# Performance work log

Hardware: AMD Instinct MI355X
Metric: run time of the kernel (lower is better)

Reference implementation:

```python
import jax, jax.numpy as jnp
import numpy as np

B, N, C, H = 4, 1024, 1024, 16
D = C // H  # head_dim = 64


def setup_inputs() -> dict:
    key = jax.random.key(0)
    k1, k2, k3 = jax.random.split(key, 3)
    x = jax.random.normal(k1, (B, N, C), dtype=jnp.float32)
    Wqkv = jax.random.normal(k2, (3 * C, C), dtype=jnp.float32) * (C ** -0.5)
    Wproj = jax.random.normal(k3, (C, C), dtype=jnp.float32) * (C ** -0.5)
    bproj = jnp.zeros((C,), dtype=jnp.float32)
    epoch = 25  # selects mask_2 (window w=8) per the original branching
    return {"x": x, "Wqkv": Wqkv, "Wproj": Wproj, "bproj": bproj, "epoch": epoch}


def _band_mask(n, w):
    # get_attn_mask(N, w) == (|i - j| <= w) for every row (boundary cases included)
    idx = jnp.arange(n)
    return jnp.abs(idx[:, None] - idx[None, :]) <= w


def reference(x, Wqkv, Wproj, bproj, epoch):
    b, n, c = x.shape
    d = c // H
    # qkv linear (no bias), then the module's per-head interleaved split:
    # view(B,N,H,3d) -> permute(B,H,N,3d) -> tensor_split into q,k,v
    qkv = jnp.einsum('bnc,oc->bno', x, Wqkv)            # [B,N,3C]
    qkv = qkv.reshape(b, n, H, 3 * d).transpose(0, 2, 1, 3)  # [B,H,N,3d]
    q, k, v = jnp.split(qkv, 3, axis=-1)                # each [B,H,N,d]
    scale = d ** -0.5
    score = jnp.einsum('bhid,bhjd->bhij', q, k) * scale  # [B,H,N,N]
    if epoch is not None and epoch < 50:
        if epoch < 20:
            w = 6
        elif epoch < 30:
            w = 8
        elif epoch < 40:
            w = 10
        else:
            w = 12
        mask = _band_mask(n, w)  # [N,N] bool
        score = jnp.where(mask[None, None], score, jnp.float32(-1e9))
    attn = jax.nn.softmax(score, axis=-1)
    ctx = jnp.einsum('bhij,bhjd->bhid', attn, v)         # [B,H,N,d]
    ctx = ctx.transpose(0, 2, 1, 3).reshape(b, n, c)     # [B,N,C]
    out = jnp.einsum('bnc,oc->bno', ctx, Wproj) + bproj
    return out
```

## Files before the change

### kernel.cpp

```cpp
#include <hip/hip_runtime.h>
#include <hip/hip_bf16.h>


typedef __bf16 bf16x8_t __attribute__((ext_vector_type(8)));
typedef unsigned short u16x8_t __attribute__((ext_vector_type(8)));
typedef float f32x4_t __attribute__((ext_vector_type(4)));

__device__ __forceinline__ void load_lds16(const void* g, void* l) {
    __builtin_amdgcn_global_load_lds(
        (__attribute__((address_space(1))) void*)(g),
        (__attribute__((address_space(3))) void*)(l),
        16, 0, 0);
}

__device__ __forceinline__ u16x8_t cvt8(float4 u, float4 v) {
    union { u16x8_t p; __hip_bfloat16 h[8]; } w;
    w.h[0] = __float2bfloat16(u.x); w.h[1] = __float2bfloat16(u.y);
    w.h[2] = __float2bfloat16(u.z); w.h[3] = __float2bfloat16(u.w);
    w.h[4] = __float2bfloat16(v.x); w.h[5] = __float2bfloat16(v.y);
    w.h[6] = __float2bfloat16(v.z); w.h[7] = __float2bfloat16(v.w);
    return w.p;
}

__global__ __launch_bounds__(512, 2) void gemm1_qkv(
    const float* __restrict__ A,
    const float* __restrict__ B,
    __hip_bfloat16* __restrict__ C)
{
    __shared__ __align__(16) char smem[114688];
    const int tid = threadIdx.x;

    const int orig = blockIdx.y * 16 + blockIdx.x;
    const int xcd = orig & 7, slot = orig >> 3;
    const int hi = slot >> 4;
    const int s  = xcd * 2 + hi;
    const int w  = slot & 15;
    const int m0 = ((s & 3) * 4 + (w & 3)) * 256;
    const int n0 = ((s >> 2) * 4 + (w >> 2)) * 192;

    const int wave = tid >> 6, lane = tid & 63;
    const int wr = wave >> 2, wc = wave & 3;
    const int lr = lane & 15, kg = lane >> 4;
    const int K = 1024, Nn = 3072;

    const int qa0 = tid, qa1 = tid + 512;
    const int qb0 = tid, qb1 = tid + 256;
    const int ra0 = qa0 >> 2, ca0 = ((qa0 & 3) ^ ((ra0 >> 1) & 3)) * 8;
    const int ra1 = qa1 >> 2, ca1 = ((qa1 & 3) ^ ((ra1 >> 1) & 3)) * 8;
    const int rb0 = qb0 >> 2, cb0 = ((qb0 & 3) ^ ((rb0 >> 1) & 3)) * 8;
    const int rb1 = qb1 >> 2, cb1 = ((qb1 & 3) ^ ((rb1 >> 1) & 3)) * 8;
    const float* Ap0 = A + (size_t)(m0 + ra0) * K + ca0;
    const float* Ap1 = A + (size_t)(m0 + ra1) * K + ca1;
    const float* Bp0 = B + (size_t)(n0 + rb0) * K + cb0;
    const float* Bp1 = B + (size_t)(n0 + rb1) * K + cb1;
    const bool bextra = (tid >= 256);

    float4 a00 = {}, a01 = {}, a10 = {}, a11 = {};
    float4 b00 = {}, b01 = {}, b10 = {}, b11 = {};

#define LOADR(t) { const int ko_ = (t) * 32;                                   \
    a00 = *(const float4*)(Ap0 + ko_); a01 = *(const float4*)(Ap0 + ko_ + 4);  \
    a10 = *(const float4*)(Ap1 + ko_); a11 = *(const float4*)(Ap1 + ko_ + 4);  \
    b00 = *(const float4*)(Bp0 + ko_); b01 = *(const float4*)(Bp0 + ko_ + 4);  \
    if (bextra) { b10 = *(const float4*)(Bp1 + ko_);                           \
                  b11 = *(const float4*)(Bp1 + ko_ + 4); } }
#define WRITE(t) { char* d_ = smem + ((t) & 3) * 28672;                        \
    *(u16x8_t*)(d_ + qa0 * 16) = cvt8(a00, a01);                               \
    *(u16x8_t*)(d_ + qa1 * 16) = cvt8(a10, a11);                               \
    *(u16x8_t*)(d_ + 16384 + qb0 * 16) = cvt8(b00, b01);                       \
    if (bextra) *(u16x8_t*)(d_ + 16384 + qb1 * 16) = cvt8(b10, b11); }

    f32x4_t acc[8][3] = {};
    const int rsw = ((kg ^ ((lr >> 1) & 3)) * 16);
    const int arow = wr * 128 + lr;
    const int brow = wc * 48 + lr;

    LOADR(0); WRITE(0);
    LOADR(1); WRITE(1);
    LOADR(2);
    __syncthreads();

    for (int t = 0; t < 32; ++t) {
        const int sb_ = (t & 3) * 28672;
        bf16x8_t a_[8], b_[3];
#pragma unroll
        for (int mi = 0; mi < 8; ++mi)
            a_[mi] = *(const bf16x8_t*)(smem + sb_ + (arow + mi * 16) * 64 + rsw);
#pragma unroll
        for (int ni = 0; ni < 3; ++ni)
            b_[ni] = *(const bf16x8_t*)(smem + sb_ + 16384 + (brow + ni * 16) * 64 + rsw);
        if (t < 30) WRITE(t + 2);
        if (t < 29) LOADR(t + 3);
        __builtin_amdgcn_s_setprio(1);
#pragma unroll
        for (int mi = 0; mi < 8; ++mi)
#pragma unroll
            for (int ni = 0; ni < 3; ++ni)
                acc[mi][ni] = __builtin_amdgcn_mfma_f32_16x16x32_bf16(
                    a_[mi], b_[ni], acc[mi][ni], 0, 0, 0);
        __builtin_amdgcn_s_setprio(0);
        __syncthreads();
    }
#undef LOADR
#undef WRITE

    __hip_bfloat16* cl = (__hip_bfloat16*)smem;
#pragma unroll
    for (int mi = 0; mi < 8; ++mi)
#pragma unroll
        for (int ni = 0; ni < 3; ++ni)
#pragma unroll
            for (int r = 0; r < 4; ++r)
                cl[(wr * 128 + mi * 16 + kg * 4 + r) * 200 + wc * 48 + ni * 16 + lr] =
                    __float2bfloat16(acc[mi][ni][r]);
    __syncthreads();
#pragma unroll
    for (int c = 0; c < 12; ++c) {
        const int id = tid + c * 512;
        const int row = id / 24, cc = id - row * 24;
        f32x4_t v = *(const f32x4_t*)(smem + row * 400 + cc * 16);
        *(f32x4_t*)((char*)C + ((size_t)(m0 + row) * Nn + n0) * 2 + cc * 16) = v;
    }
}

__global__ __launch_bounds__(512, 2) void gemm2_proj(
    const __hip_bfloat16* __restrict__ A,
    const float* __restrict__ B,
    float* __restrict__ C,
    const float* __restrict__ bias)
{
    __shared__ __align__(16) char smem[65536];
    const int tid = threadIdx.x;
    const int orig = blockIdx.y * 8 + blockIdx.x;
    const int wgid = (orig & 7) * 32 + (orig >> 3);
    const int m0 = (wgid >> 3) * 128, n0 = (wgid & 7) * 128;

    const int wave = tid >> 6, lane = tid & 63;
    const int wr = wave >> 2, wc = wave & 3;
    const int lr = lane & 15, kg = lane >> 4;
    const int K = 1024, Nn = 1024;

    const int q = tid;
    const int row = q >> 2, cw = ((q & 3) ^ ((row >> 1) & 3)) * 8;
    const __hip_bfloat16* Ap = A + (size_t)(m0 + row) * K + cw;
    const float*          Bp = B + (size_t)(n0 + row) * K + cw;

    float4 av = {}, bv0 = {}, bv1 = {};

#define LOADR2(t) { const int ko_ = (t) * 32;                                  \
    av  = *(const float4*)(Ap + ko_);                        \
    bv0 = *(const float4*)(Bp + ko_); bv1 = *(const float4*)(Bp + ko_ + 4); }
#define WRITE2(t) { char* d_ = smem + ((t) & 3) * 16384;                       \
    *(float4*)(d_ + q * 16) = av;                                              \
    *(u16x8_t*)(d_ + 8192 + q * 16) = cvt8(bv0, bv1); }

    f32x4_t acc[4][2] = {};
    const int rsw = ((kg ^ ((lr >> 1) & 3)) * 16);
    const int arow = wr * 64 + lr;
    const int brow = wc * 32 + lr;

    LOADR2(0); WRITE2(0);
    LOADR2(1); WRITE2(1);
    LOADR2(2);
    __syncthreads();

    for (int t = 0; t < 32; ++t) {
        const int sb_ = (t & 3) * 16384;
        bf16x8_t a_[4], b_[2];
#pragma unroll
        for (int mi = 0; mi < 4; ++mi)
            a_[mi] = *(const bf16x8_t*)(smem + sb_ + (arow + mi * 16) * 64 + rsw);
#pragma unroll
        for (int ni = 0; ni < 2; ++ni)
            b_[ni] = *(const bf16x8_t*)(smem + sb_ + 8192 + (brow + ni * 16) * 64 + rsw);
        if (t < 30) WRITE2(t + 2);
        if (t < 29) LOADR2(t + 3);
        __builtin_amdgcn_s_setprio(1);
#pragma unroll
        for (int mi = 0; mi < 4; ++mi)
#pragma unroll
            for (int ni = 0; ni < 2; ++ni)
                acc[mi][ni] = __builtin_amdgcn_mfma_f32_16x16x32_bf16(
                    a_[mi], b_[ni], acc[mi][ni], 0, 0, 0);
        __builtin_amdgcn_s_setprio(0);
        __syncthreads();
    }
#undef LOADR2
#undef WRITE2

    float* cf = (float*)smem;
#pragma unroll
    for (int p = 0; p < 2; ++p) {
        if (p) __syncthreads();
        if (wr == p) {
#pragma unroll
            for (int mi = 0; mi < 4; ++mi)
#pragma unroll
                for (int ni = 0; ni < 2; ++ni) {
                    const int scol = wc * 32 + ni * 16 + lr;
#pragma unroll
                    for (int r = 0; r < 4; ++r)
                        cf[(mi * 16 + kg * 4 + r) * 132 + scol] = acc[mi][ni][r];
                }
        }
        __syncthreads();
#pragma unroll
        for (int cc = 0; cc < 4; ++cc) {
            const int chunk = tid + cc * 512;
            const int srow = chunk >> 5;
            const int sc = (chunk & 31) * 4;
            f32x4_t v = *(const f32x4_t*)(smem + srow * 528 + sc * 4);
            const f32x4_t bv = *(const f32x4_t*)(bias + n0 + sc);
            v += bv;
            *(f32x4_t*)(C + (size_t)(m0 + p * 64 + srow) * Nn + n0 + sc) = v;
        }
    }
}

__global__ __launch_bounds__(256) void attn_band_mfma(
    const __hip_bfloat16* __restrict__ qkv,
    __hip_bfloat16* __restrict__ ctx,
    const int* __restrict__ epoch_ptr)
{
    __shared__ __align__(16) __hip_bfloat16 K_lds[128 * 64];
    __shared__ __align__(16) __hip_bfloat16 V_lds[64 * 136];
    __shared__ __hip_bfloat16 P_lds[4][16 * 40];

    const int tid = threadIdx.x;
    const int wave = tid >> 6, lane = tid & 63;
    const int lr = lane & 15, kg = lane >> 4;

    const int bid = blockIdx.x;
    const int tg = bid & 15;
    const int bh = bid >> 4;
    const int h = bh & 15, b = bh >> 4;
    const int base = tg * 64;
    const int i0 = base + wave * 16;

    const int e = *epoch_ptr;
    int w;
    if      (e < 20) w = 6;
    else if (e < 30) w = 8;
    else if (e < 40) w = 10;
    else if (e < 50) w = 12;
    else             w = 1023;

    const size_t rowb = (size_t)b * 1024;
    const int hq = h * 192;

#pragma unroll
    for (int it = 0; it < 4; ++it) {
        const int q = tid + it * 256;
        const int row = q >> 3, s = q & 7;
        const int c = s ^ (row & 7);
        int gk = base - 32 + row;
        gk = gk < 0 ? 0 : (gk > 1023 ? 1023 : gk);
        load_lds16(qkv + (rowb + gk) * 3072 + hq + 64 + c * 8,
                   (char*)K_lds + q * 16);
    }
    {
        const int pr = tid & 63, dg = tid >> 6;
        int gk0 = base - 32 + 2 * pr, gk1 = gk0 + 1;
        gk0 = gk0 < 0 ? 0 : (gk0 > 1023 ? 1023 : gk0);
        gk1 = gk1 < 0 ? 0 : (gk1 > 1023 ? 1023 : gk1);
        const __hip_bfloat16* v0 = qkv + (rowb + gk0) * 3072 + hq + 128 + dg * 16;
        const __hip_bfloat16* v1 = qkv + (rowb + gk1) * 3072 + hq + 128 + dg * 16;
        u16x8_t a0 = *(const u16x8_t*)v0, b0 = *(const u16x8_t*)(v0 + 8);
        u16x8_t a1 = *(const u16x8_t*)v1, b1 = *(const u16x8_t*)(v1 + 8);
#pragma unroll
        for (int c2 = 0; c2 < 8; ++c2) {
            *(unsigned int*)&V_lds[(dg * 16 + c2) * 136 + 2 * pr] =
                (unsigned int)a0[c2] | ((unsigned int)a1[c2] << 16);
            *(unsigned int*)&V_lds[(dg * 16 + 8 + c2) * 136 + 2 * pr] =
                (unsigned int)b0[c2] | ((unsigned int)b1[c2] << 16);
        }
    }

    bf16x8_t aq[2];
#pragma unroll
    for (int ks = 0; ks < 2; ++ks)
        aq[ks] = *(const bf16x8_t*)(qkv + (rowb + i0 + lr) * 3072 + hq + ks * 32 + kg * 8);

    __syncthreads();

    float m[4] = {-1e30f, -1e30f, -1e30f, -1e30f};
    float l[4] = {0.f, 0.f, 0.f, 0.f};
    f32x4_t o[4] = {};

    int jlo = i0 - w;      if (jlo < 0) jlo = 0;
    int jhi = i0 + 15 + w; if (jhi > 1023) jhi = 1023;
    const int t0 = (base >> 5) - 1;

    for (int p = (jlo >> 5); p <= (jhi >> 5); ++p) {
        const int kb = p * 32;
        const int tl = p - t0;

        f32x4_t s2[2] = {};
#pragma unroll
        for (int t = 0; t < 2; ++t)
#pragma unroll
            for (int ks = 0; ks < 2; ++ks) {
                const int lkr = tl * 32 + t * 16 + lr;
                bf16x8_t bk = *(const bf16x8_t*)(
                    (char*)K_lds + lkr * 128 + (((ks * 4 + kg) ^ (lr & 7)) * 16));
                s2[t] = __builtin_amdgcn_mfma_f32_16x16x32_bf16(aq[ks], bk, s2[t], 0, 0, 0);
            }

        float sv[2][4];
#pragma unroll
        for (int t = 0; t < 2; ++t)
#pragma unroll
            for (int r = 0; r < 4; ++r) {
                const int qi = i0 + kg * 4 + r;
                const int j  = kb + t * 16 + lr;
                int d = qi - j; if (d < 0) d = -d;
                sv[t][r] = (d <= w) ? s2[t][r] * 0.125f : -1e30f;
            }

        float tm[4];
#pragma unroll
        for (int r = 0; r < 4; ++r) tm[r] = fmaxf(sv[0][r], sv[1][r]);
#pragma unroll
        for (int msk = 1; msk < 16; msk <<= 1)
#pragma unroll
            for (int r = 0; r < 4; ++r) tm[r] = fmaxf(tm[r], __shfl_xor(tm[r], msk));

        float sc[4], ps[4], pvv[2][4];
#pragma unroll
        for (int r = 0; r < 4; ++r) {
            const float mn = fmaxf(m[r], tm[r]);
            sc[r] = __expf(m[r] - mn);
            pvv[0][r] = __expf(sv[0][r] - mn);
            pvv[1][r] = __expf(sv[1][r] - mn);
            ps[r] = pvv[0][r] + pvv[1][r];
            m[r] = mn;
        }
#pragma unroll
        for (int msk = 1; msk < 16; msk <<= 1)
#pragma unroll
            for (int r = 0; r < 4; ++r) ps[r] += __shfl_xor(ps[r], msk);
#pragma unroll
        for (int r = 0; r < 4; ++r) l[r] = l[r] * sc[r] + ps[r];
#pragma unroll
        for (int ni = 0; ni < 4; ++ni)
#pragma unroll
            for (int r = 0; r < 4; ++r) o[ni][r] *= sc[r];

#pragma unroll
        for (int t = 0; t < 2; ++t)
#pragma unroll
            for (int r = 0; r < 4; ++r)
                P_lds[wave][(kg * 4 + r) * 40 + t * 16 + lr] =
                    __float2bfloat16(pvv[t][r]);

        bf16x8_t ap = *(const bf16x8_t*)&P_lds[wave][lr * 40 + kg * 8];
#pragma unroll
        for (int ni = 0; ni < 4; ++ni) {
            bf16x8_t bv = *(const bf16x8_t*)&V_lds[(ni * 16 + lr) * 136 + tl * 32 + kg * 8];
            o[ni] = __builtin_amdgcn_mfma_f32_16x16x32_bf16(ap, bv, o[ni], 0, 0, 0);
        }
    }

#pragma unroll
    for (int ni = 0; ni < 4; ++ni)
#pragma unroll
        for (int r = 0; r < 4; ++r)
            ctx[(rowb + i0 + kg * 4 + r) * 1024 + h * 64 + ni * 16 + lr] =
                __float2bfloat16(o[ni][r] / l[r]);
}

extern "C" void kernel_launch(void* const* d_in, const int* in_sizes, int n_in,
                              void* d_out, int out_size, void* d_ws, size_t ws_size,
                              hipStream_t stream)
{
    const float* x     = (const float*)d_in[0];
    const float* Wqkv  = (const float*)d_in[1];
    const float* Wproj = (const float*)d_in[2];
    const float* bproj = (const float*)d_in[3];
    const int*   epoch = (const int*)d_in[4];

    char* ws = (char*)d_ws;
    __hip_bfloat16* qkvb = (__hip_bfloat16*)(ws);
    __hip_bfloat16* ctxb = (__hip_bfloat16*)(ws + 25165824);

    gemm1_qkv<<<dim3(16, 16), 512, 0, stream>>>(x, Wqkv, qkvb);

    attn_band_mfma<<<1024, 256, 0, stream>>>(qkvb, ctxb, epoch);

    gemm2_proj<<<dim3(8, 32), 512, 0, stream>>>(
        ctxb, Wproj, (float*)d_out, bproj);
}
```

Before: 68.05 us.

## Double K-tile depth to 64 in both GEMMs with double-buffered LDS

Both GEMM kernels now stage K-tiles of 64 instead of 32. The LDS ring goes from four stages to two, with an 8-way XOR swizzle over 128-byte rows, and each tile is consumed in two 32-wide MFMA sub-steps. This halves the number of __syncthreads barriers and main-loop iterations and issues larger batches of global loads, at the cost of more registers held for prefetched data and a shallower prefetch pipeline. The projection output store also becomes nontemporal.

Result: slower. 83.91 us (+23.3%).

```diff
diff --git a/kernel.cpp b/kernel.cpp
--- a/kernel.cpp
+++ b/kernel.cpp
@@ -43,62 +43,68 @@
     const int lr = lane & 15, kg = lane >> 4;
     const int K = 1024, Nn = 3072;
 
-    const int qa0 = tid, qa1 = tid + 512;
-    const int qb0 = tid, qb1 = tid + 256;
-    const int ra0 = qa0 >> 2, ca0 = ((qa0 & 3) ^ ((ra0 >> 1) & 3)) * 8;
-    const int ra1 = qa1 >> 2, ca1 = ((qa1 & 3) ^ ((ra1 >> 1) & 3)) * 8;
-    const int rb0 = qb0 >> 2, cb0 = ((qb0 & 3) ^ ((rb0 >> 1) & 3)) * 8;
-    const int rb1 = qb1 >> 2, cb1 = ((qb1 & 3) ^ ((rb1 >> 1) & 3)) * 8;
-    const float* Ap0 = A + (size_t)(m0 + ra0) * K + ca0;
-    const float* Ap1 = A + (size_t)(m0 + ra1) * K + ca1;
-    const float* Bp0 = B + (size_t)(n0 + rb0) * K + cb0;
-    const float* Bp1 = B + (size_t)(n0 + rb1) * K + cb1;
-    const bool bextra = (tid >= 256);
-
-    float4 a00 = {}, a01 = {}, a10 = {}, a11 = {};
-    float4 b00 = {}, b01 = {}, b10 = {}, b11 = {};
-
-#define LOADR(t) { const int ko_ = (t) * 32;                                   \
-    a00 = *(const float4*)(Ap0 + ko_); a01 = *(const float4*)(Ap0 + ko_ + 4);  \
-    a10 = *(const float4*)(Ap1 + ko_); a11 = *(const float4*)(Ap1 + ko_ + 4);  \
-    b00 = *(const float4*)(Bp0 + ko_); b01 = *(const float4*)(Bp0 + ko_ + 4);  \
-    if (bextra) { b10 = *(const float4*)(Bp1 + ko_);                           \
-                  b11 = *(const float4*)(Bp1 + ko_ + 4); } }
-#define WRITE(t) { char* d_ = smem + ((t) & 3) * 28672;                        \
-    *(u16x8_t*)(d_ + qa0 * 16) = cvt8(a00, a01);                               \
-    *(u16x8_t*)(d_ + qa1 * 16) = cvt8(a10, a11);                               \
-    *(u16x8_t*)(d_ + 16384 + qb0 * 16) = cvt8(b00, b01);                       \
-    if (bextra) *(u16x8_t*)(d_ + 16384 + qb1 * 16) = cvt8(b10, b11); }
+    const float* ApP[4];
+    const float* BpP[3];
+#pragma unroll
+    for (int i = 0; i < 4; ++i) {
+        const int q = tid + i * 512, row = q >> 3, c = (q & 7) ^ (row & 7);
+        ApP[i] = A + (size_t)(m0 + row) * K + c * 8;
+    }
+#pragma unroll
+    for (int i = 0; i < 3; ++i) {
+        const int q = tid + i * 512, row = q >> 3, c = (q & 7) ^ (row & 7);
+        BpP[i] = B + (size_t)(n0 + row) * K + c * 8;
+    }
+
+    float4 sa[4][2], sb[3][2];
+
+#define LOADR(t) { const int ko_ = (t) * 64;                                    \
+    _Pragma("unroll") for (int i = 0; i < 4; ++i) {                             \
+        sa[i][0] = *(const float4*)(ApP[i] + ko_);                              \
+        sa[i][1] = *(const float4*)(ApP[i] + ko_ + 4); }                        \
+    _Pragma("unroll") for (int i = 0; i < 3; ++i) {                             \
+        sb[i][0] = *(const float4*)(BpP[i] + ko_);                              \
+        sb[i][1] = *(const float4*)(BpP[i] + ko_ + 4); } }
+#define WRITE(t) { char* d_ = smem + ((t) & 1) * 57344;                         \
+    _Pragma("unroll") for (int i = 0; i < 4; ++i)                               \
+        *(u16x8_t*)(d_ + (tid + i * 512) * 16) = cvt8(sa[i][0], sa[i][1]);      \
+    _Pragma("unroll") for (int i = 0; i < 3; ++i)                               \
+        *(u16x8_t*)(d_ + 32768 + (tid + i * 512) * 16) = cvt8(sb[i][0], sb[i][1]); }
 
     f32x4_t acc[8][3] = {};
-    const int rsw = ((kg ^ ((lr >> 1) & 3)) * 16);
     const int arow = wr * 128 + lr;
     const int brow = wc * 48 + lr;
 
     LOADR(0); WRITE(0);
-    LOADR(1); WRITE(1);
-    LOADR(2);
+    LOADR(1);
     __syncthreads();
 
-    for (int t = 0; t < 32; ++t) {
-        const int sb_ = (t & 3) * 28672;
-        bf16x8_t a_[8], b_[3];
-#pragma unroll
-        for (int mi = 0; mi < 8; ++mi)
-            a_[mi] = *(const bf16x8_t*)(smem + sb_ + (arow + mi * 16) * 64 + rsw);
-#pragma unroll
-        for (int ni = 0; ni < 3; ++ni)
-            b_[ni] = *(const bf16x8_t*)(smem + sb_ + 16384 + (brow + ni * 16) * 64 + rsw);
-        if (t < 30) WRITE(t + 2);
-        if (t < 29) LOADR(t + 3);
-        __builtin_amdgcn_s_setprio(1);
-#pragma unroll
-        for (int mi = 0; mi < 8; ++mi)
+    for (int t = 0; t < 16; ++t) {
+        const int sb_ = (t & 1) * 57344;
+#pragma unroll
+        for (int ks = 0; ks < 2; ++ks) {
+            const int ch = ((kg + ks * 4) ^ (lr & 7)) * 16;
+            bf16x8_t aF[8], bF[3];
+#pragma unroll
+            for (int mi = 0; mi < 8; ++mi)
+                aF[mi] = *(const bf16x8_t*)(smem + sb_ + (arow + mi * 16) * 128 + ch);
 #pragma unroll
             for (int ni = 0; ni < 3; ++ni)
-                acc[mi][ni] = __builtin_amdgcn_mfma_f32_16x16x32_bf16(
-                    a_[mi], b_[ni], acc[mi][ni], 0, 0, 0);
-        __builtin_amdgcn_s_setprio(0);
+                bF[ni] = *(const bf16x8_t*)(smem + sb_ + 32768 + (brow + ni * 16) * 128 + ch);
+            if (ks == 0) {
+                if (t < 15) WRITE(t + 1);
+            } else {
+                if (t < 14) LOADR(t + 2);
+            }
+            __builtin_amdgcn_s_setprio(1);
+#pragma unroll
+            for (int mi = 0; mi < 8; ++mi)
+#pragma unroll
+                for (int ni = 0; ni < 3; ++ni)
+                    acc[mi][ni] = __builtin_amdgcn_mfma_f32_16x16x32_bf16(
+                        aF[mi], bF[ni], acc[mi][ni], 0, 0, 0);
+            __builtin_amdgcn_s_setprio(0);
+        }
         __syncthreads();
     }
 #undef LOADR
@@ -140,49 +146,61 @@
     const int lr = lane & 15, kg = lane >> 4;
     const int K = 1024, Nn = 1024;
 
-    const int q = tid;
-    const int row = q >> 2, cw = ((q & 3) ^ ((row >> 1) & 3)) * 8;
-    const __hip_bfloat16* Ap = A + (size_t)(m0 + row) * K + cw;
-    const float*          Bp = B + (size_t)(n0 + row) * K + cw;
-
-    float4 av = {}, bv0 = {}, bv1 = {};
-
-#define LOADR2(t) { const int ko_ = (t) * 32;                                  \
-    av  = *(const float4*)(Ap + ko_);                        \
-    bv0 = *(const float4*)(Bp + ko_); bv1 = *(const float4*)(Bp + ko_ + 4); }
-#define WRITE2(t) { char* d_ = smem + ((t) & 3) * 16384;                       \
-    *(float4*)(d_ + q * 16) = av;                                              \
-    *(u16x8_t*)(d_ + 8192 + q * 16) = cvt8(bv0, bv1); }
+    const __hip_bfloat16* ApP[2];
+    const float* BpP[2];
+#pragma unroll
+    for (int i = 0; i < 2; ++i) {
+        const int q = tid + i * 512, row = q >> 3, c = (q & 7) ^ (row & 7);
+        ApP[i] = A + (size_t)(m0 + row) * K + c * 8;
+        BpP[i] = B + (size_t)(n0 + row) * K + c * 8;
+    }
+
+    float4 sa[2], sbl[2][2];
+
+#define LOADR2(t) { const int ko_ = (t) * 64;                                   \
+    _Pragma("unroll") for (int i = 0; i < 2; ++i) {                             \
+        sa[i] = *(const float4*)(ApP[i] + ko_);                                 \
+        sbl[i][0] = *(const float4*)(BpP[i] + ko_);                             \
+        sbl[i][1] = *(const float4*)(BpP[i] + ko_ + 4); } }
+#define WRITE2(t) { char* d_ = smem + ((t) & 1) * 32768;                        \
+    _Pragma("unroll") for (int i = 0; i < 2; ++i) {                             \
+        *(float4*)(d_ + (tid + i * 512) * 16) = sa[i];                          \
+        *(u16x8_t*)(d_ + 16384 + (tid + i * 512) * 16) = cvt8(sbl[i][0], sbl[i][1]); } }
 
     f32x4_t acc[4][2] = {};
-    const int rsw = ((kg ^ ((lr >> 1) & 3)) * 16);
     const int arow = wr * 64 + lr;
     const int brow = wc * 32 + lr;
 
     LOADR2(0); WRITE2(0);
-    LOADR2(1); WRITE2(1);
-    LOADR2(2);
+    LOADR2(1);
     __syncthreads();
 
-    for (int t = 0; t < 32; ++t) {
-        const int sb_ = (t & 3) * 16384;
-        bf16x8_t a_[4], b_[2];
-#pragma unroll
-        for (int mi = 0; mi < 4; ++mi)
-            a_[mi] = *(const bf16x8_t*)(smem + sb_ + (arow + mi * 16) * 64 + rsw);
-#pragma unroll
-        for (int ni = 0; ni < 2; ++ni)
-            b_[ni] = *(const bf16x8_t*)(smem + sb_ + 8192 + (brow + ni * 16) * 64 + rsw);
-        if (t < 30) WRITE2(t + 2);
-        if (t < 29) LOADR2(t + 3);
-        __builtin_amdgcn_s_setprio(1);
-#pragma unroll
-        for (int mi = 0; mi < 4; ++mi)
+    for (int t = 0; t < 16; ++t) {
+        const int sb_ = (t & 1) * 32768;
+#pragma unroll
+        for (int ks = 0; ks < 2; ++ks) {
+            const int ch = ((kg + ks * 4) ^ (lr & 7)) * 16;
+            bf16x8_t aF[4], bF[2];
+#pragma unroll
+            for (int mi = 0; mi < 4; ++mi)
+                aF[mi] = *(const bf16x8_t*)(smem + sb_ + (arow + mi * 16) * 128 + ch);
 #pragma unroll
             for (int ni = 0; ni < 2; ++ni)
-                acc[mi][ni] = __builtin_amdgcn_mfma_f32_16x16x32_bf16(
-                    a_[mi], b_[ni], acc[mi][ni], 0, 0, 0);
-        __builtin_amdgcn_s_setprio(0);
+                bF[ni] = *(const bf16x8_t*)(smem + sb_ + 16384 + (brow + ni * 16) * 128 + ch);
+            if (ks == 0) {
+                if (t < 15) WRITE2(t + 1);
+            } else {
+                if (t < 14) LOADR2(t + 2);
+            }
+            __builtin_amdgcn_s_setprio(1);
+#pragma unroll
+            for (int mi = 0; mi < 4; ++mi)
+#pragma unroll
+                for (int ni = 0; ni < 2; ++ni)
+                    acc[mi][ni] = __builtin_amdgcn_mfma_f32_16x16x32_bf16(
+                        aF[mi], bF[ni], acc[mi][ni], 0, 0, 0);
+            __builtin_amdgcn_s_setprio(0);
+        }
         __syncthreads();
     }
 #undef LOADR2
@@ -212,7 +230,8 @@
             f32x4_t v = *(const f32x4_t*)(smem + srow * 528 + sc * 4);
             const f32x4_t bv = *(const f32x4_t*)(bias + n0 + sc);
             v += bv;
-            *(f32x4_t*)(C + (size_t)(m0 + p * 64 + srow) * Nn + n0 + sc) = v;
+            __builtin_nontemporal_store(
+                v, (f32x4_t*)(C + (size_t)(m0 + p * 64 + srow) * Nn + n0 + sc));
         }
     }
 }
```

## Fuse QKV GEMM, banded attention and projection into one cooperative persistent kernel

Applied to the files above, without the earlier changes.

Merges the three kernels into a single cooperative launch of 256 blocks of 512 threads, separated by grid-wide syncs. The attention stage is remapped so that each 512-thread block runs two 256-thread sub-groups, each handling two attention tiles over two iterations. The goal is to remove the launch gaps and tail effects between kernels. In exchange it adds two grid barriers, gives attention fewer but larger blocks, and forces all stages to share the large GEMM1 LDS footprint, which may limit occupancy.

Result: slower. 242.3 us (+256.0%).

```diff
diff --git a/kernel.cpp b/kernel.cpp
--- a/kernel.cpp
+++ b/kernel.cpp
@@ -1,5 +1,8 @@
 #include <hip/hip_runtime.h>
 #include <hip/hip_bf16.h>
+#include <hip/hip_cooperative_groups.h>
+
+namespace cg = cooperative_groups;
 
 
 typedef __bf16 bf16x8_t __attribute__((ext_vector_type(8)));
@@ -22,41 +25,49 @@
     return w.p;
 }
 
-__global__ __launch_bounds__(512, 2) void gemm1_qkv(
-    const float* __restrict__ A,
-    const float* __restrict__ B,
-    __hip_bfloat16* __restrict__ C)
+__global__ __launch_bounds__(512, 2) void fused_all(
+    const float* __restrict__ x,
+    const float* __restrict__ Wqkv,
+    const float* __restrict__ Wproj,
+    const float* __restrict__ bproj,
+    const int* __restrict__ epoch_ptr,
+    __hip_bfloat16* __restrict__ qkv,
+    __hip_bfloat16* __restrict__ ctx,
+    float* __restrict__ out)
 {
     __shared__ __align__(16) char smem[114688];
+    cg::grid_group grid = cg::this_grid();
     const int tid = threadIdx.x;
-
-    const int orig = blockIdx.y * 16 + blockIdx.x;
-    const int xcd = orig & 7, slot = orig >> 3;
-    const int hi = slot >> 4;
-    const int s  = xcd * 2 + hi;
-    const int w  = slot & 15;
-    const int m0 = ((s & 3) * 4 + (w & 3)) * 256;
-    const int n0 = ((s >> 2) * 4 + (w >> 2)) * 192;
-
-    const int wave = tid >> 6, lane = tid & 63;
-    const int wr = wave >> 2, wc = wave & 3;
+    const int pb = blockIdx.x;
+    const int lane = tid & 63;
     const int lr = lane & 15, kg = lane >> 4;
-    const int K = 1024, Nn = 3072;
-
-    const int qa0 = tid, qa1 = tid + 512;
-    const int qb0 = tid, qb1 = tid + 256;
-    const int ra0 = qa0 >> 2, ca0 = ((qa0 & 3) ^ ((ra0 >> 1) & 3)) * 8;
-    const int ra1 = qa1 >> 2, ca1 = ((qa1 & 3) ^ ((ra1 >> 1) & 3)) * 8;
-    const int rb0 = qb0 >> 2, cb0 = ((qb0 & 3) ^ ((rb0 >> 1) & 3)) * 8;
-    const int rb1 = qb1 >> 2, cb1 = ((qb1 & 3) ^ ((rb1 >> 1) & 3)) * 8;
-    const float* Ap0 = A + (size_t)(m0 + ra0) * K + ca0;
-    const float* Ap1 = A + (size_t)(m0 + ra1) * K + ca1;
-    const float* Bp0 = B + (size_t)(n0 + rb0) * K + cb0;
-    const float* Bp1 = B + (size_t)(n0 + rb1) * K + cb1;
-    const bool bextra = (tid >= 256);
-
-    float4 a00 = {}, a01 = {}, a10 = {}, a11 = {};
-    float4 b00 = {}, b01 = {}, b10 = {}, b11 = {};
+
+    {
+        const int xcd = pb & 7, slot = pb >> 3;
+        const int hi = slot >> 4;
+        const int s  = xcd * 2 + hi;
+        const int w  = slot & 15;
+        const int m0 = ((s & 3) * 4 + (w & 3)) * 256;
+        const int n0 = ((s >> 2) * 4 + (w >> 2)) * 192;
+
+        const int wave = tid >> 6;
+        const int wr = wave >> 2, wc = wave & 3;
+        const int K = 1024, Nn = 3072;
+
+        const int qa0 = tid, qa1 = tid + 512;
+        const int qb0 = tid, qb1 = tid + 256;
+        const int ra0 = qa0 >> 2, ca0 = ((qa0 & 3) ^ ((ra0 >> 1) & 3)) * 8;
+        const int ra1 = qa1 >> 2, ca1 = ((qa1 & 3) ^ ((ra1 >> 1) & 3)) * 8;
+        const int rb0 = qb0 >> 2, cb0 = ((qb0 & 3) ^ ((rb0 >> 1) & 3)) * 8;
+        const int rb1 = qb1 >> 2, cb1 = ((qb1 & 3) ^ ((rb1 >> 1) & 3)) * 8;
+        const float* Ap0 = x + (size_t)(m0 + ra0) * K + ca0;
+        const float* Ap1 = x + (size_t)(m0 + ra1) * K + ca1;
+        const float* Bp0 = Wqkv + (size_t)(n0 + rb0) * K + cb0;
+        const float* Bp1 = Wqkv + (size_t)(n0 + rb1) * K + cb1;
+        const bool bextra = (tid >= 256);
+
+        float4 a00 = {}, a01 = {}, a10 = {}, a11 = {};
+        float4 b00 = {}, b01 = {}, b10 = {}, b11 = {};
 
 #define LOADR(t) { const int ko_ = (t) * 32;                                   \
     a00 = *(const float4*)(Ap0 + ko_); a01 = *(const float4*)(Ap0 + ko_ + 4);  \
@@ -70,303 +81,302 @@
     *(u16x8_t*)(d_ + 16384 + qb0 * 16) = cvt8(b00, b01);                       \
     if (bextra) *(u16x8_t*)(d_ + 16384 + qb1 * 16) = cvt8(b10, b11); }
 
-    f32x4_t acc[8][3] = {};
-    const int rsw = ((kg ^ ((lr >> 1) & 3)) * 16);
-    const int arow = wr * 128 + lr;
-    const int brow = wc * 48 + lr;
-
-    LOADR(0); WRITE(0);
-    LOADR(1); WRITE(1);
-    LOADR(2);
-    __syncthreads();
-
-    for (int t = 0; t < 32; ++t) {
-        const int sb_ = (t & 3) * 28672;
-        bf16x8_t a_[8], b_[3];
-#pragma unroll
-        for (int mi = 0; mi < 8; ++mi)
-            a_[mi] = *(const bf16x8_t*)(smem + sb_ + (arow + mi * 16) * 64 + rsw);
-#pragma unroll
-        for (int ni = 0; ni < 3; ++ni)
-            b_[ni] = *(const bf16x8_t*)(smem + sb_ + 16384 + (brow + ni * 16) * 64 + rsw);
-        if (t < 30) WRITE(t + 2);
-        if (t < 29) LOADR(t + 3);
-        __builtin_amdgcn_s_setprio(1);
-#pragma unroll
-        for (int mi = 0; mi < 8; ++mi)
+        f32x4_t acc[8][3] = {};
+        const int rsw = ((kg ^ ((lr >> 1) & 3)) * 16);
+        const int arow = wr * 128 + lr;
+        const int brow = wc * 48 + lr;
+
+        LOADR(0); WRITE(0);
+        LOADR(1); WRITE(1);
+        LOADR(2);
+        __syncthreads();
+
+        for (int t = 0; t < 32; ++t) {
+            const int sb_ = (t & 3) * 28672;
+            bf16x8_t a_[8], b_[3];
+#pragma unroll
+            for (int mi = 0; mi < 8; ++mi)
+                a_[mi] = *(const bf16x8_t*)(smem + sb_ + (arow + mi * 16) * 64 + rsw);
 #pragma unroll
             for (int ni = 0; ni < 3; ++ni)
-                acc[mi][ni] = __builtin_amdgcn_mfma_f32_16x16x32_bf16(
-                    a_[mi], b_[ni], acc[mi][ni], 0, 0, 0);
-        __builtin_amdgcn_s_setprio(0);
-        __syncthreads();
-    }
+                b_[ni] = *(const bf16x8_t*)(smem + sb_ + 16384 + (brow + ni * 16) * 64 + rsw);
+            if (t < 30) WRITE(t + 2);
+            if (t < 29) LOADR(t + 3);
+            __builtin_amdgcn_s_setprio(1);
+#pragma unroll
+            for (int mi = 0; mi < 8; ++mi)
+#pragma unroll
+                for (int ni = 0; ni < 3; ++ni)
+                    acc[mi][ni] = __builtin_amdgcn_mfma_f32_16x16x32_bf16(
+                        a_[mi], b_[ni], acc[mi][ni], 0, 0, 0);
+            __builtin_amdgcn_s_setprio(0);
+            __syncthreads();
+        }
 #undef LOADR
 #undef WRITE
 
-    __hip_bfloat16* cl = (__hip_bfloat16*)smem;
-#pragma unroll
-    for (int mi = 0; mi < 8; ++mi)
-#pragma unroll
-        for (int ni = 0; ni < 3; ++ni)
-#pragma unroll
-            for (int r = 0; r < 4; ++r)
-                cl[(wr * 128 + mi * 16 + kg * 4 + r) * 200 + wc * 48 + ni * 16 + lr] =
-                    __float2bfloat16(acc[mi][ni][r]);
+        __hip_bfloat16* cl = (__hip_bfloat16*)smem;
+#pragma unroll
+        for (int mi = 0; mi < 8; ++mi)
+#pragma unroll
+            for (int ni = 0; ni < 3; ++ni)
+#pragma unroll
+                for (int r = 0; r < 4; ++r)
+                    cl[(wr * 128 + mi * 16 + kg * 4 + r) * 200 + wc * 48 + ni * 16 + lr] =
+                        __float2bfloat16(acc[mi][ni][r]);
+        __syncthreads();
+#pragma unroll
+        for (int c = 0; c < 12; ++c) {
+            const int id = tid + c * 512;
+            const int row = id / 24, cc = id - row * 24;
+            f32x4_t v = *(const f32x4_t*)(smem + row * 400 + cc * 16);
+            *(f32x4_t*)((char*)qkv + ((size_t)(m0 + row) * Nn + n0) * 2 + cc * 16) = v;
+        }
+    }
+
     __syncthreads();
-#pragma unroll
-    for (int c = 0; c < 12; ++c) {
-        const int id = tid + c * 512;
-        const int row = id / 24, cc = id - row * 24;
-        f32x4_t v = *(const f32x4_t*)(smem + row * 400 + cc * 16);
-        *(f32x4_t*)((char*)C + ((size_t)(m0 + row) * Nn + n0) * 2 + cc * 16) = v;
+    __threadfence();
+    grid.sync();
+
+    {
+        const int e = *epoch_ptr;
+        int wband;
+        if      (e < 20) wband = 6;
+        else if (e < 30) wband = 8;
+        else if (e < 40) wband = 10;
+        else if (e < 50) wband = 12;
+        else             wband = 1023;
+
+        const int g = tid >> 8;
+        const int t256 = tid & 255;
+        const int wave4 = (tid >> 6) & 3;
+        char* base = smem + g * 38912;
+        __hip_bfloat16* K_lds = (__hip_bfloat16*)base;
+        __hip_bfloat16* V_lds = (__hip_bfloat16*)(base + 16384);
+        __hip_bfloat16* P_w   = (__hip_bfloat16*)(base + 33792) + wave4 * 640;
+
+        for (int it2 = 0; it2 < 2; ++it2) {
+            __syncthreads();
+            const int lb = pb * 4 + it2 * 2 + g;
+            const int tg = lb & 15;
+            const int bh = lb >> 4;
+            const int h = bh & 15, b = bh >> 4;
+            const int baseq = tg * 64;
+            const int i0 = baseq + wave4 * 16;
+            const size_t rowb = (size_t)b * 1024;
+            const int hq = h * 192;
+
+#pragma unroll
+            for (int it = 0; it < 4; ++it) {
+                const int q = t256 + it * 256;
+                const int row = q >> 3, s = q & 7;
+                const int c = s ^ (row & 7);
+                int gk = baseq - 32 + row;
+                gk = gk < 0 ? 0 : (gk > 1023 ? 1023 : gk);
+                load_lds16(qkv + (rowb + gk) * 3072 + hq + 64 + c * 8,
+                           (char*)K_lds + q * 16);
+            }
+            {
+                const int pr = t256 & 63, dg = t256 >> 6;
+                int gk0 = baseq - 32 + 2 * pr, gk1 = gk0 + 1;
+                gk0 = gk0 < 0 ? 0 : (gk0 > 1023 ? 1023 : gk0);
+                gk1 = gk1 < 0 ? 0 : (gk1 > 1023 ? 1023 : gk1);
+                const __hip_bfloat16* v0 = qkv + (rowb + gk0) * 3072 + hq + 128 + dg * 16;
+                const __hip_bfloat16* v1 = qkv + (rowb + gk1) * 3072 + hq + 128 + dg * 16;
+                u16x8_t a0 = *(const u16x8_t*)v0, b0 = *(const u16x8_t*)(v0 + 8);
+                u16x8_t a1 = *(const u16x8_t*)v1, b1 = *(const u16x8_t*)(v1 + 8);
+#pragma unroll
+                for (int c2 = 0; c2 < 8; ++c2) {
+                    *(unsigned int*)&V_lds[(dg * 16 + c2) * 136 + 2 * pr] =
+                        (unsigned int)a0[c2] | ((unsigned int)a1[c2] << 16);
+                    *(unsigned int*)&V_lds[(dg * 16 + 8 + c2) * 136 + 2 * pr] =
+                        (unsigned int)b0[c2] | ((unsigned int)b1[c2] << 16);
+                }
+            }
+
+            bf16x8_t aq[2];
+#pragma unroll
+            for (int ks = 0; ks < 2; ++ks)
+                aq[ks] = *(const bf16x8_t*)(qkv + (rowb + i0 + lr) * 3072 + hq + ks * 32 + kg * 8);
+
+            __syncthreads();
+
+            float m[4] = {-1e30f, -1e30f, -1e30f, -1e30f};
+            float l[4] = {0.f, 0.f, 0.f, 0.f};
+            f32x4_t o[4] = {};
+
+            int jlo = i0 - wband;      if (jlo < 0) jlo = 0;
+            int jhi = i0 + 15 + wband; if (jhi > 1023) jhi = 1023;
+            const int t0 = (baseq >> 5) - 1;
+
+            for (int p = (jlo >> 5); p <= (jhi >> 5); ++p) {
+                const int kb = p * 32;
+                const int tl = p - t0;
+
+                f32x4_t s2[2] = {};
+#pragma unroll
+                for (int t = 0; t < 2; ++t)
+#pragma unroll
+                    for (int ks = 0; ks < 2; ++ks) {
+                        const int lkr = tl * 32 + t * 16 + lr;
+                        bf16x8_t bk = *(const bf16x8_t*)(
+                            (char*)K_lds + lkr * 128 + (((ks * 4 + kg) ^ (lr & 7)) * 16));
+                        s2[t] = __builtin_amdgcn_mfma_f32_16x16x32_bf16(aq[ks], bk, s2[t], 0, 0, 0);
+                    }
+
+                float sv[2][4];
+#pragma unroll
+                for (int t = 0; t < 2; ++t)
+#pragma unroll
+                    for (int r = 0; r < 4; ++r) {
+                        const int qi = i0 + kg * 4 + r;
+                        const int j  = kb + t * 16 + lr;
+                        int d = qi - j; if (d < 0) d = -d;
+                        sv[t][r] = (d <= wband) ? s2[t][r] * 0.125f : -1e30f;
+                    }
+
+                float tm[4];
+#pragma unroll
+                for (int r = 0; r < 4; ++r) tm[r] = fmaxf(sv[0][r], sv[1][r]);
+#pragma unroll
+                for (int msk = 1; msk < 16; msk <<= 1)
+#pragma unroll
+                    for (int r = 0; r < 4; ++r) tm[r] = fmaxf(tm[r], __shfl_xor(tm[r], msk));
+
+                float sc[4], ps[4], pvv[2][4];
+#pragma unroll
+                for (int r = 0; r < 4; ++r) {
+                    const float mn = fmaxf(m[r], tm[r]);
+                    sc[r] = __expf(m[r] - mn);
+                    pvv[0][r] = __expf(sv[0][r] - mn);
+                    pvv[1][r] = __expf(sv[1][r] - mn);
+                    ps[r] = pvv[0][r] + pvv[1][r];
+                    m[r] = mn;
+                }
+#pragma unroll
+                for (int msk = 1; msk < 16; msk <<= 1)
+#pragma unroll
+                    for (int r = 0; r < 4; ++r) ps[r] += __shfl_xor(ps[r], msk);
+#pragma unroll
+                for (int r = 0; r < 4; ++r) l[r] = l[r] * sc[r] + ps[r];
+#pragma unroll
+                for (int ni = 0; ni < 4; ++ni)
+#pragma unroll
+                    for (int r = 0; r < 4; ++r) o[ni][r] *= sc[r];
+
+#pragma unroll
+                for (int t = 0; t < 2; ++t)
+#pragma unroll
+                    for (int r = 0; r < 4; ++r)
+                        P_w[(kg * 4 + r) * 40 + t * 16 + lr] =
+                            __float2bfloat16(pvv[t][r]);
+
+                bf16x8_t ap = *(const bf16x8_t*)&P_w[lr * 40 + kg * 8];
+#pragma unroll
+                for (int ni = 0; ni < 4; ++ni) {
+                    bf16x8_t bv = *(const bf16x8_t*)&V_lds[(ni * 16 + lr) * 136 + tl * 32 + kg * 8];
+                    o[ni] = __builtin_amdgcn_mfma_f32_16x16x32_bf16(ap, bv, o[ni], 0, 0, 0);
+                }
+            }
+
+#pragma unroll
+            for (int ni = 0; ni < 4; ++ni)
+#pragma unroll
+                for (int r = 0; r < 4; ++r)
+                    ctx[(rowb + i0 + kg * 4 + r) * 1024 + h * 64 + ni * 16 + lr] =
+                        __float2bfloat16(o[ni][r] / l[r]);
+        }
     }
-}
-
-__global__ __launch_bounds__(512, 2) void gemm2_proj(
-    const __hip_bfloat16* __restrict__ A,
-    const float* __restrict__ B,
-    float* __restrict__ C,
-    const float* __restrict__ bias)
-{
-    __shared__ __align__(16) char smem[65536];
-    const int tid = threadIdx.x;
-    const int orig = blockIdx.y * 8 + blockIdx.x;
-    const int wgid = (orig & 7) * 32 + (orig >> 3);
-    const int m0 = (wgid >> 3) * 128, n0 = (wgid & 7) * 128;
-
-    const int wave = tid >> 6, lane = tid & 63;
-    const int wr = wave >> 2, wc = wave & 3;
-    const int lr = lane & 15, kg = lane >> 4;
-    const int K = 1024, Nn = 1024;
-
-    const int q = tid;
-    const int row = q >> 2, cw = ((q & 3) ^ ((row >> 1) & 3)) * 8;
-    const __hip_bfloat16* Ap = A + (size_t)(m0 + row) * K + cw;
-    const float*          Bp = B + (size_t)(n0 + row) * K + cw;
-
-    float4 av = {}, bv0 = {}, bv1 = {};
+
+    __syncthreads();
+    __threadfence();
+    grid.sync();
+
+    {
+        const int wgid = (pb & 7) * 32 + (pb >> 3);
+        const int m0 = (wgid >> 3) * 128, n0 = (wgid & 7) * 128;
+
+        const int wave = tid >> 6;
+        const int wr = wave >> 2, wc = wave & 3;
+        const int K = 1024, Nn = 1024;
+
+        const int q = tid;
+        const int row = q >> 2, cw = ((q & 3) ^ ((row >> 1) & 3)) * 8;
+        const __hip_bfloat16* Ap = ctx + (size_t)(m0 + row) * K + cw;
+        const float*          Bp = Wproj + (size_t)(n0 + row) * K + cw;
+
+        float4 av = {}, bv0 = {}, bv1 = {};
 
 #define LOADR2(t) { const int ko_ = (t) * 32;                                  \
-    av  = *(const float4*)(Ap + ko_);                        \
+    av  = *(const float4*)(Ap + ko_);                                          \
     bv0 = *(const float4*)(Bp + ko_); bv1 = *(const float4*)(Bp + ko_ + 4); }
 #define WRITE2(t) { char* d_ = smem + ((t) & 3) * 16384;                       \
     *(float4*)(d_ + q * 16) = av;                                              \
     *(u16x8_t*)(d_ + 8192 + q * 16) = cvt8(bv0, bv1); }
 
-    f32x4_t acc[4][2] = {};
-    const int rsw = ((kg ^ ((lr >> 1) & 3)) * 16);
-    const int arow = wr * 64 + lr;
-    const int brow = wc * 32 + lr;
-
-    LOADR2(0); WRITE2(0);
-    LOADR2(1); WRITE2(1);
-    LOADR2(2);
-    __syncthreads();
-
-    for (int t = 0; t < 32; ++t) {
-        const int sb_ = (t & 3) * 16384;
-        bf16x8_t a_[4], b_[2];
-#pragma unroll
-        for (int mi = 0; mi < 4; ++mi)
-            a_[mi] = *(const bf16x8_t*)(smem + sb_ + (arow + mi * 16) * 64 + rsw);
-#pragma unroll
-        for (int ni = 0; ni < 2; ++ni)
-            b_[ni] = *(const bf16x8_t*)(smem + sb_ + 8192 + (brow + ni * 16) * 64 + rsw);
-        if (t < 30) WRITE2(t + 2);
-        if (t < 29) LOADR2(t + 3);
-        __builtin_amdgcn_s_setprio(1);
-#pragma unroll
-        for (int mi = 0; mi < 4; ++mi)
+        f32x4_t acc[4][2] = {};
+        const int rsw = ((kg ^ ((lr >> 1) & 3)) * 16);
+        const int arow = wr * 64 + lr;
+        const int brow = wc * 32 + lr;
+
+        __syncthreads();
+        LOADR2(0); WRITE2(0);
+        LOADR2(1); WRITE2(1);
+        LOADR2(2);
+        __syncthreads();
+
+        for (int t = 0; t < 32; ++t) {
+            const int sb_ = (t & 3) * 16384;
+            bf16x8_t a_[4], b_[2];
+#pragma unroll
+            for (int mi = 0; mi < 4; ++mi)
+                a_[mi] = *(const bf16x8_t*)(smem + sb_ + (arow + mi * 16) * 64 + rsw);
 #pragma unroll
             for (int ni = 0; ni < 2; ++ni)
-                acc[mi][ni] = __builtin_amdgcn_mfma_f32_16x16x32_bf16(
-                    a_[mi], b_[ni], acc[mi][ni], 0, 0, 0);
-        __builtin_amdgcn_s_setprio(0);
-        __syncthreads();
-    }
+                b_[ni] = *(const bf16x8_t*)(smem + sb_ + 8192 + (brow + ni * 16) * 64 + rsw);
+            if (t < 30) WRITE2(t + 2);
+            if (t < 29) LOADR2(t + 3);
+            __builtin_amdgcn_s_setprio(1);
+#pragma unroll
+            for (int mi = 0; mi < 4; ++mi)
+#pragma unroll
+                for (int ni = 0; ni < 2; ++ni)
+                    acc[mi][ni] = __builtin_amdgcn_mfma_f32_16x16x32_bf16(
+                        a_[mi], b_[ni], acc[mi][ni], 0, 0, 0);
+            __builtin_amdgcn_s_setprio(0);
+            __syncthreads();
+        }
 #undef LOADR2
 #undef WRITE2
 
-    float* cf = (float*)smem;
-#pragma unroll
-    for (int p = 0; p < 2; ++p) {
-        if (p) __syncthreads();
-        if (wr == p) {
-#pragma unroll
-            for (int mi = 0; mi < 4; ++mi)
-#pragma unroll
-                for (int ni = 0; ni < 2; ++ni) {
-                    const int scol = wc * 32 + ni * 16 + lr;
-#pragma unroll
-                    for (int r = 0; r < 4; ++r)
-                        cf[(mi * 16 + kg * 4 + r) * 132 + scol] = acc[mi][ni][r];
-                }
-        }
-        __syncthreads();
-#pragma unroll
-        for (int cc = 0; cc < 4; ++cc) {
-            const int chunk = tid + cc * 512;
-            const int srow = chunk >> 5;
-            const int sc = (chunk & 31) * 4;
-            f32x4_t v = *(const f32x4_t*)(smem + srow * 528 + sc * 4);
-            const f32x4_t bv = *(const f32x4_t*)(bias + n0 + sc);
-            v += bv;
-            *(f32x4_t*)(C + (size_t)(m0 + p * 64 + srow) * Nn + n0 + sc) = v;
+        float* cf = (float*)smem;
+#pragma unroll
+        for (int p = 0; p < 2; ++p) {
+            if (p) __syncthreads();
+            if (wr == p) {
+#pragma unroll
+                for (int mi = 0; mi < 4; ++mi)
+#pragma unroll
+                    for (int ni = 0; ni < 2; ++ni) {
+                        const int scol = wc * 32 + ni * 16 + lr;
+#pragma unroll
+                        for (int r = 0; r < 4; ++r)
+                            cf[(mi * 16 + kg * 4 + r) * 132 + scol] = acc[mi][ni][r];
+                    }
+            }
+            __syncthreads();
+#pragma unroll
+            for (int cc = 0; cc < 4; ++cc) {
+                const int chunk = tid + cc * 512;
+                const int srow = chunk >> 5;
+                const int sc = (chunk & 31) * 4;
+                f32x4_t v = *(const f32x4_t*)(smem + srow * 528 + sc * 4);
+                const f32x4_t bv = *(const f32x4_t*)(bproj + n0 + sc);
+                v += bv;
+                *(f32x4_t*)(out + (size_t)(m0 + p * 64 + srow) * Nn + n0 + sc) = v;
+            }
         }
     }
-}
-
-__global__ __launch_bounds__(256) void attn_band_mfma(
-    const __hip_bfloat16* __restrict__ qkv,
-    __hip_bfloat16* __restrict__ ctx,
-    const int* __restrict__ epoch_ptr)
-{
-    __shared__ __align__(16) __hip_bfloat16 K_lds[128 * 64];
-    __shared__ __align__(16) __hip_bfloat16 V_lds[64 * 136];
-    __shared__ __hip_bfloat16 P_lds[4][16 * 40];
-
-    const int tid = threadIdx.x;
-    const int wave = tid >> 6, lane = tid & 63;
-    const int lr = lane & 15, kg = lane >> 4;
-
-    const int bid = blockIdx.x;
-    const int tg = bid & 15;
-    const int bh = bid >> 4;
-    const int h = bh & 15, b = bh >> 4;
-    const int base = tg * 64;
-    const int i0 = base + wave * 16;
-
-    const int e = *epoch_ptr;
-    int w;
-    if      (e < 20) w = 6;
-    else if (e < 30) w = 8;
-    else if (e < 40) w = 10;
-    else if (e < 50) w = 12;
-    else             w = 1023;
-
-    const size_t rowb = (size_t)b * 1024;
-    const int hq = h * 192;
-
-#pragma unroll
-    for (int it = 0; it < 4; ++it) {
-        const int q = tid + it * 256;
-        const int row = q >> 3, s = q & 7;
-        const int c = s ^ (row & 7);
-        int gk = base - 32 + row;
-        gk = gk < 0 ? 0 : (gk > 1023 ? 1023 : gk);
-        load_lds16(qkv + (rowb + gk) * 3072 + hq + 64 + c * 8,
-                   (char*)K_lds + q * 16);
-    }
-    {
-        const int pr = tid & 63, dg = tid >> 6;
-        int gk0 = base - 32 + 2 * pr, gk1 = gk0 + 1;
-        gk0 = gk0 < 0 ? 0 : (gk0 > 1023 ? 1023 : gk0);
-        gk1 = gk1 < 0 ? 0 : (gk1 > 1023 ? 1023 : gk1);
-        const __hip_bfloat16* v0 = qkv + (rowb + gk0) * 3072 + hq + 128 + dg * 16;
-        const __hip_bfloat16* v1 = qkv + (rowb + gk1) * 3072 + hq + 128 + dg * 16;
-        u16x8_t a0 = *(const u16x8_t*)v0, b0 = *(const u16x8_t*)(v0 + 8);
-        u16x8_t a1 = *(const u16x8_t*)v1, b1 = *(const u16x8_t*)(v1 + 8);
-#pragma unroll
-        for (int c2 = 0; c2 < 8; ++c2) {
-            *(unsigned int*)&V_lds[(dg * 16 + c2) * 136 + 2 * pr] =
-                (unsigned int)a0[c2] | ((unsigned int)a1[c2] << 16);
-            *(unsigned int*)&V_lds[(dg * 16 + 8 + c2) * 136 + 2 * pr] =
-                (unsigned int)b0[c2] | ((unsigned int)b1[c2] << 16);
-        }
-    }
-
-    bf16x8_t aq[2];
-#pragma unroll
-    for (int ks = 0; ks < 2; ++ks)
-        aq[ks] = *(const bf16x8_t*)(qkv + (rowb + i0 + lr) * 3072 + hq + ks * 32 + kg * 8);
-
-    __syncthreads();
-
-    float m[4] = {-1e30f, -1e30f, -1e30f, -1e30f};
-    float l[4] = {0.f, 0.f, 0.f, 0.f};
-    f32x4_t o[4] = {};
-
-    int jlo = i0 - w;      if (jlo < 0) jlo = 0;
-    int jhi = i0 + 15 + w; if (jhi > 1023) jhi = 1023;
-    const int t0 = (base >> 5) - 1;
-
-    for (int p = (jlo >> 5); p <= (jhi >> 5); ++p) {
-        const int kb = p * 32;
-        const int tl = p - t0;
-
-        f32x4_t s2[2] = {};
-#pragma unroll
-        for (int t = 0; t < 2; ++t)
-#pragma unroll
-            for (int ks = 0; ks < 2; ++ks) {
-                const int lkr = tl * 32 + t * 16 + lr;
-                bf16x8_t bk = *(const bf16x8_t*)(
-                    (char*)K_lds + lkr * 128 + (((ks * 4 + kg) ^ (lr & 7)) * 16));
-                s2[t] = __builtin_amdgcn_mfma_f32_16x16x32_bf16(aq[ks], bk, s2[t], 0, 0, 0);
-            }
-
-        float sv[2][4];
-#pragma unroll
-        for (int t = 0; t < 2; ++t)
-#pragma unroll
-            for (int r = 0; r < 4; ++r) {
-                const int qi = i0 + kg * 4 + r;
-                const int j  = kb + t * 16 + lr;
-                int d = qi - j; if (d < 0) d = -d;
-                sv[t][r] = (d <= w) ? s2[t][r] * 0.125f : -1e30f;
-            }
-
-        float tm[4];
-#pragma unroll
-        for (int r = 0; r < 4; ++r) tm[r] = fmaxf(sv[0][r], sv[1][r]);
-#pragma unroll
-        for (int msk = 1; msk < 16; msk <<= 1)
-#pragma unroll
-            for (int r = 0; r < 4; ++r) tm[r] = fmaxf(tm[r], __shfl_xor(tm[r], msk));
-
-        float sc[4], ps[4], pvv[2][4];
-#pragma unroll
-        for (int r = 0; r < 4; ++r) {
-            const float mn = fmaxf(m[r], tm[r]);
-            sc[r] = __expf(m[r] - mn);
-            pvv[0][r] = __expf(sv[0][r] - mn);
-            pvv[1][r] = __expf(sv[1][r] - mn);
-            ps[r] = pvv[0][r] + pvv[1][r];
-            m[r] = mn;
-        }
-#pragma unroll
-        for (int msk = 1; msk < 16; msk <<= 1)
-#pragma unroll
-            for (int r = 0; r < 4; ++r) ps[r] += __shfl_xor(ps[r], msk);
-#pragma unroll
-        for (int r = 0; r < 4; ++r) l[r] = l[r] * sc[r] + ps[r];
-#pragma unroll
-        for (int ni = 0; ni < 4; ++ni)
-#pragma unroll
-            for (int r = 0; r < 4; ++r) o[ni][r] *= sc[r];
-
-#pragma unroll
-        for (int t = 0; t < 2; ++t)
-#pragma unroll
-            for (int r = 0; r < 4; ++r)
-                P_lds[wave][(kg * 4 + r) * 40 + t * 16 + lr] =
-                    __float2bfloat16(pvv[t][r]);
-
-        bf16x8_t ap = *(const bf16x8_t*)&P_lds[wave][lr * 40 + kg * 8];
-#pragma unroll
-        for (int ni = 0; ni < 4; ++ni) {
-            bf16x8_t bv = *(const bf16x8_t*)&V_lds[(ni * 16 + lr) * 136 + tl * 32 + kg * 8];
-            o[ni] = __builtin_amdgcn_mfma_f32_16x16x32_bf16(ap, bv, o[ni], 0, 0, 0);
-        }
-    }
-
-#pragma unroll
-    for (int ni = 0; ni < 4; ++ni)
-#pragma unroll
-        for (int r = 0; r < 4; ++r)
-            ctx[(rowb + i0 + kg * 4 + r) * 1024 + h * 64 + ni * 16 + lr] =
-                __float2bfloat16(o[ni][r] / l[r]);
 }
 
 extern "C" void kernel_launch(void* const* d_in, const int* in_sizes, int n_in,
@@ -382,11 +392,10 @@
     char* ws = (char*)d_ws;
     __hip_bfloat16* qkvb = (__hip_bfloat16*)(ws);
     __hip_bfloat16* ctxb = (__hip_bfloat16*)(ws + 25165824);
-
-    gemm1_qkv<<<dim3(16, 16), 512, 0, stream>>>(x, Wqkv, qkvb);
-
-    attn_band_mfma<<<1024, 256, 0, stream>>>(qkvb, ctxb, epoch);
-
-    gemm2_proj<<<dim3(8, 32), 512, 0, stream>>>(
-        ctxb, Wproj, (float*)d_out, bproj);
+    float* outp = (float*)d_out;
+
+    void* kargs[] = { (void*)&x, (void*)&Wqkv, (void*)&Wproj, (void*)&bproj,
+                      (void*)&epoch, (void*)&qkvb, (void*)&ctxb, (void*)&outp };
+    hipLaunchCooperativeKernel((const void*)fused_all, dim3(256), dim3(512),
+                               kargs, 0, stream);
 }
```
